# Kernel optimization log

Hardware: AMD Instinct MI355X
Metric: run time of the kernel (lower is better)

## Reference

```python
import jax, jax.numpy as jnp
import numpy as np

N, E, P = 50000, 800000, 500000
NODE_IN, HIDDEN, EDGE_IN = 128, 256, 16


def setup_inputs() -> dict:
    key = jax.random.key(0)
    ks = jax.random.split(key, 16)
    s = lambda k, shape, fan_in: jax.random.normal(k, shape, jnp.float32) * (1.0 / np.sqrt(fan_in))
    return {
        "x": jax.random.normal(ks[0], (N, NODE_IN), jnp.float32),
        "edge_index": jax.random.randint(ks[1], (2, E), 0, N),
        "edge_u": jax.random.randint(ks[2], (P,), 0, N),
        "edge_v": jax.random.randint(ks[3], (P,), 0, N),
        "edge_attr": jax.random.normal(ks[4], (P, EDGE_IN), jnp.float32),
        "log_exposure": jax.random.normal(ks[5], (P,), jnp.float32),
        # conv1: lin_l (on mean-aggregated neighbors, with bias), lin_r (on root, no bias)
        "Wl1": s(ks[6], (HIDDEN, NODE_IN), NODE_IN),
        "bl1": jnp.zeros((HIDDEN,), jnp.float32),
        "Wr1": s(ks[7], (HIDDEN, NODE_IN), NODE_IN),
        # conv2
        "Wl2": s(ks[8], (HIDDEN, HIDDEN), HIDDEN),
        "bl2": jnp.zeros((HIDDEN,), jnp.float32),
        "Wr2": s(ks[9], (HIDDEN, HIDDEN), HIDDEN),
        # edge MLP: Linear(2*hidden+edge_in, hidden) -> ReLU -> Linear(hidden, 1)
        "W1": s(ks[10], (HIDDEN, 2 * HIDDEN + EDGE_IN), 2 * HIDDEN + EDGE_IN),
        "b1": jnp.zeros((HIDDEN,), jnp.float32),
        "W2": s(ks[11], (1, HIDDEN), HIDDEN),
        "b2": jnp.zeros((1,), jnp.float32),
    }


def sage_conv(x, src, dst, Wl, bl, Wr):
    # PyG SAGEConv, mean aggregation: out = lin_l(mean_{j in N(i)} x_j) + lin_r(x_i)
    n = x.shape[0]
    agg = jax.ops.segment_sum(x[src], dst, num_segments=n)          # [N, F]
    cnt = jax.ops.segment_sum(jnp.ones((src.shape[0],), x.dtype), dst, num_segments=n)
    agg = agg / jnp.maximum(cnt, 1.0)[:, None]
    return agg @ Wl.T + bl + x @ Wr.T


def reference(x, edge_index, edge_u, edge_v, edge_attr, log_exposure,
              Wl1, bl1, Wr1, Wl2, bl2, Wr2, W1, b1, W2, b2):
    src, dst = edge_index[0], edge_index[1]
    # eval mode: dropout is identity
    h = jax.nn.relu(sage_conv(x, src, dst, Wl1, bl1, Wr1))
    h = jax.nn.relu(sage_conv(h, src, dst, Wl2, bl2, Wr2))
    z = jnp.concatenate([h[edge_u], h[edge_v], edge_attr], axis=1)  # [P, 2H+Ein]
    s = (jax.nn.relu(z @ W1.T + b1) @ W2.T + b2)[:, 0]              # [P]
    return log_exposure + s
```

## Files before the change

kernel.cpp:

```cpp
#include <hip/hip_runtime.h>


typedef float f32x4 __attribute__((ext_vector_type(4)));
typedef float f32x2 __attribute__((ext_vector_type(2)));
typedef __bf16 bf16x8 __attribute__((ext_vector_type(8)));

__device__ __forceinline__ unsigned short f2b(float f) {
    unsigned u = __float_as_uint(f);
    u = u + 0x7fffu + ((u >> 16) & 1u);
    return (unsigned short)(u >> 16);
}
__device__ __forceinline__ float b2f(unsigned short s) {
    return __uint_as_float(((unsigned)s) << 16);
}
__device__ __forceinline__ float blo(unsigned x) { return b2f((unsigned short)(x & 0xffffu)); }
__device__ __forceinline__ float bhi(unsigned x) { return b2f((unsigned short)(x >> 16)); }
__device__ __forceinline__ unsigned padd(unsigned a, unsigned b) {
    float lo = __uint_as_float(a << 16) + __uint_as_float(b << 16);
    float hi = __uint_as_float(a & 0xffff0000u) + __uint_as_float(b & 0xffff0000u);
    return (__float_as_uint(hi) & 0xffff0000u) | (__float_as_uint(lo) >> 16);
}
__device__ __forceinline__ int swz(int r, int g) { return (g + (r >> 1)) & 3; }
__device__ __forceinline__ unsigned char f2f8(float v) {
    return (unsigned char)(__builtin_amdgcn_cvt_pk_fp8_f32(v, v, 0, false) & 0xff);
}


__global__ void k_count(const int* __restrict__ dst, int* __restrict__ cnt, int E) {
    int e = blockIdx.x * 256 + threadIdx.x;
    if (e < E) atomicAdd(&cnt[dst[e]], 1);
}

__global__ __launch_bounds__(1024) void k_scan(int* __restrict__ cnt_cursor,
                                               int* __restrict__ row_ptr, int n) {
    __shared__ int wsum[16];
    __shared__ int carry;
    int t = threadIdx.x, lane = t & 63, w = t >> 6;
    if (t == 0) carry = 0;
    __syncthreads();
    int nch = (n + 1023) >> 10;
    for (int ch = 0; ch < nch; ++ch) {
        int i = (ch << 10) + t;
        int v = (i < n) ? cnt_cursor[i] : 0;
        int s = v;
        #pragma unroll
        for (int off = 1; off < 64; off <<= 1) {
            int u = __shfl_up(s, off);
            if (lane >= off) s += u;
        }
        if (lane == 63) wsum[w] = s;
        __syncthreads();
        int wpre = 0;
        for (int j = 0; j < w; ++j) wpre += wsum[j];
        int incl = s + wpre;
        int base = carry;
        if (i < n) { int ex = base + incl - v; row_ptr[i] = ex; cnt_cursor[i] = ex; }
        __syncthreads();
        if (t == 1023) carry = base + incl;
    }
    __syncthreads();
    if (t == 0) row_ptr[n] = carry;
}

__global__ void k_scatter(const int* __restrict__ src, const int* __restrict__ dst,
                          int* __restrict__ cursor, int* __restrict__ bucket, int E) {
    int e = blockIdx.x * 256 + threadIdx.x;
    if (e < E) {
        int p = atomicAdd(&cursor[dst[e]], 1);
        bucket[p] = src[e];
    }
}


__global__ void k_convert_weights(const float* __restrict__ Wl1, const float* __restrict__ Wr1,
                                  const float* __restrict__ Wl2, const float* __restrict__ Wr2,
                                  const float* __restrict__ W1, const float* __restrict__ b1,
                                  unsigned short* __restrict__ Wc1,
                                  unsigned short* __restrict__ Wc2,
                                  unsigned short* __restrict__ W1g,
                                  unsigned short* __restrict__ WaF) {
    int idx = blockIdx.x * 256 + threadIdx.x;
    if (idx < 65536) {
        int c = idx >> 13, j = (idx >> 5) & 255, kk = idx & 31;
        float v = (c < 4) ? Wl1[j * 128 + c * 32 + kk] : Wr1[j * 128 + (c - 4) * 32 + kk];
        Wc1[idx] = f2b(v);
    } else if (idx < 65536 + 131072) {
        int i2 = idx - 65536;
        int c = i2 >> 13, j = (i2 >> 5) & 255, kk = i2 & 31;
        float v = (c < 8) ? Wl2[j * 256 + c * 32 + kk] : Wr2[j * 256 + (c - 8) * 32 + kk];
        Wc2[i2] = f2b(v);
    } else if (idx < 65536 + 131072 + 131072) {
        int i3 = idx - 65536 - 131072;
        int c = i3 >> 14, j = (i3 >> 5) & 511, kk = i3 & 31;
        float v = (j < 256) ? W1[(size_t)j * 528 + c * 32 + kk]
                            : W1[(size_t)(j - 256) * 528 + 256 + c * 32 + kk];
        W1g[i3] = f2b(v);
    } else if (idx < 65536 + 131072 + 131072 + 8192) {
        int i4 = idx - 65536 - 131072 - 131072;
        int mi = i4 >> 9, l = (i4 >> 3) & 63, j = i4 & 7;
        int m = mi * 16 + (l & 15);
        int k = (l >> 4) * 8 + j;
        float v = (k < 16) ? W1[(size_t)m * 528 + 512 + k] : (k == 16 ? b1[m] : 0.f);
        WaF[i4] = f2b(v);
    }
}

__global__ void k_xconvert(const float* __restrict__ in, unsigned short* __restrict__ xb,
                           unsigned char* __restrict__ xf8, int n) {
    int j = (blockIdx.x * 256 + threadIdx.x) * 2;
    if (j < n) {
        float a = in[j], b = in[j + 1];
        xb[j] = f2b(a); xb[j + 1] = f2b(b);
        unsigned p = __builtin_amdgcn_cvt_pk_fp8_f32(a, b, 0, false);
        *reinterpret_cast<unsigned short*>(xf8 + j) = (unsigned short)(p & 0xffffu);
    }
}


__device__ __forceinline__ void accf8(uint2 v, float* s) {
    f32x2 p0 = __builtin_amdgcn_cvt_pk_f32_fp8(v.x, false);
    f32x2 p1 = __builtin_amdgcn_cvt_pk_f32_fp8(v.x, true);
    f32x2 p2 = __builtin_amdgcn_cvt_pk_f32_fp8(v.y, false);
    f32x2 p3 = __builtin_amdgcn_cvt_pk_f32_fp8(v.y, true);
    s[0] += p0.x; s[1] += p0.y; s[2] += p1.x; s[3] += p1.y;
    s[4] += p2.x; s[5] += p2.y; s[6] += p3.x; s[7] += p3.y;
}

__global__ __launch_bounds__(256) void k_agg_x(const unsigned char* __restrict__ xf8,
                                               const int* __restrict__ row_ptr,
                                               const int* __restrict__ bucket,
                                               unsigned short* __restrict__ agg, int Nn) {
    int node = blockIdx.x * 4 + (threadIdx.x >> 6);
    if (node >= Nn) return;
    int lane = threadIdx.x & 63;
    int q = lane >> 4, c = lane & 15;
    int beg = row_ptr[node], end = row_ptr[node + 1];
    int len = end - beg;
    int lo = beg + ((len * q) >> 2);
    int hi = beg + ((len * (q + 1)) >> 2);
    float s[8] = {0.f,0.f,0.f,0.f,0.f,0.f,0.f,0.f};
    const unsigned char* xp = xf8 + c * 8;
    int e = lo;
    for (; e + 4 <= hi; e += 4) {
        int b0 = bucket[e], b1 = bucket[e + 1], b2 = bucket[e + 2], b3 = bucket[e + 3];
        uint2 v0 = *reinterpret_cast<const uint2*>(xp + (size_t)b0 * 128);
        uint2 v1 = *reinterpret_cast<const uint2*>(xp + (size_t)b1 * 128);
        uint2 v2 = *reinterpret_cast<const uint2*>(xp + (size_t)b2 * 128);
        uint2 v3 = *reinterpret_cast<const uint2*>(xp + (size_t)b3 * 128);
        accf8(v0, s); accf8(v1, s); accf8(v2, s); accf8(v3, s);
    }
    for (; e < hi; ++e)
        accf8(*reinterpret_cast<const uint2*>(xp + (size_t)bucket[e] * 128), s);
    #pragma unroll
    for (int j = 0; j < 8; ++j) {
        s[j] += __shfl_xor(s[j], 16);
        s[j] += __shfl_xor(s[j], 32);
    }
    if (q == 0) {
        float sc = 1.0f / (float)(len > 1 ? len : 1);
        uint4 o;
        o.x = (unsigned)f2b(s[0]*sc) | ((unsigned)f2b(s[1]*sc) << 16);
        o.y = (unsigned)f2b(s[2]*sc) | ((unsigned)f2b(s[3]*sc) << 16);
        o.z = (unsigned)f2b(s[4]*sc) | ((unsigned)f2b(s[5]*sc) << 16);
        o.w = (unsigned)f2b(s[6]*sc) | ((unsigned)f2b(s[7]*sc) << 16);
        *reinterpret_cast<uint4*>(agg + (size_t)node * 128 + c * 8) = o;
    }
}

__global__ __launch_bounds__(256) void k_agg_h(const unsigned char* __restrict__ hf8,
                                               const int* __restrict__ row_ptr,
                                               const int* __restrict__ bucket,
                                               unsigned short* __restrict__ agg, int Nn) {
    int node = blockIdx.x * 4 + (threadIdx.x >> 6);
    if (node >= Nn) return;
    int lane = threadIdx.x & 63;
    int g = lane >> 5, c = lane & 31;
    int beg = row_ptr[node], end = row_ptr[node + 1];
    int len = end - beg;
    int lo = beg + ((len * g) >> 1);
    int hi = beg + ((len * (g + 1)) >> 1);
    float s[8] = {0.f,0.f,0.f,0.f,0.f,0.f,0.f,0.f};
    const unsigned char* hp = hf8 + c * 8;
    int e = lo;
    for (; e + 4 <= hi; e += 4) {
        int b0 = bucket[e], b1 = bucket[e + 1], b2 = bucket[e + 2], b3 = bucket[e + 3];
        uint2 v0 = *reinterpret_cast<const uint2*>(hp + (size_t)b0 * 256);
        uint2 v1 = *reinterpret_cast<const uint2*>(hp + (size_t)b1 * 256);
        uint2 v2 = *reinterpret_cast<const uint2*>(hp + (size_t)b2 * 256);
        uint2 v3 = *reinterpret_cast<const uint2*>(hp + (size_t)b3 * 256);
        accf8(v0, s); accf8(v1, s); accf8(v2, s); accf8(v3, s);
    }
    for (; e < hi; ++e)
        accf8(*reinterpret_cast<const uint2*>(hp + (size_t)bucket[e] * 256), s);
    #pragma unroll
    for (int j = 0; j < 8; ++j) s[j] += __shfl_xor(s[j], 32);
    if (g == 0) {
        float sc = 1.0f / (float)(len > 1 ? len : 1);
        uint4 o;
        o.x = (unsigned)f2b(s[0]*sc) | ((unsigned)f2b(s[1]*sc) << 16);
        o.y = (unsigned)f2b(s[2]*sc) | ((unsigned)f2b(s[3]*sc) << 16);
        o.z = (unsigned)f2b(s[4]*sc) | ((unsigned)f2b(s[5]*sc) << 16);
        o.w = (unsigned)f2b(s[6]*sc) | ((unsigned)f2b(s[7]*sc) << 16);
        *reinterpret_cast<uint4*>(agg + (size_t)node * 256 + c * 8) = o;
    }
}


__global__ __launch_bounds__(256) void k_conv_gemm(const unsigned short* __restrict__ Aagg,
                                                   const unsigned short* __restrict__ Aself,
                                                   const unsigned short* __restrict__ Wck,
                                                   const float* __restrict__ bias,
                                                   unsigned short* __restrict__ Hout,
                                                   unsigned char* __restrict__ Hf8,
                                                   int Nn, int F) {
    __shared__ __align__(16) unsigned short zt[128 * 32];
    __shared__ __align__(16) unsigned short wt[128 * 32];
    const int t = threadIdx.x;
    const int lane = t & 63, w = t >> 6;
    const int wm = w >> 1, wn = w & 1;
    const int node0 = blockIdx.x * 128;
    const int colh = blockIdx.y;
    const int half = F >> 5, nchunks = F >> 4;

    f32x4 acc[4][4];
    #pragma unroll
    for (int i = 0; i < 4; ++i)
        #pragma unroll
        for (int j = 0; j < 4; ++j) acc[i][j] = (f32x4){0.f, 0.f, 0.f, 0.f};

    for (int c = 0; c < nchunks; ++c) {
        __syncthreads();
        const unsigned short* Asrc = (c < half) ? Aagg : Aself;
        const int ccol = ((c < half) ? c : c - half) * 32;
        #pragma unroll
        for (int p = 0; p < 2; ++p) {
            int fc = t + p * 256;
            int row = fc >> 2, seg = fc & 3;
            int node = node0 + row; if (node >= Nn) node = Nn - 1;
            uint4 v = *reinterpret_cast<const uint4*>(Asrc + (size_t)node * F + ccol + seg * 8);
            *reinterpret_cast<uint4*>(&zt[row * 32 + swz(row, seg) * 8]) = v;
        }
        const unsigned short* Wsrc = Wck + ((size_t)c * 256 + colh * 128) * 32;
        #pragma unroll
        for (int p = 0; p < 2; ++p) {
            int fc = t + p * 256;
            int row = fc >> 2, seg = fc & 3;
            *reinterpret_cast<uint4*>(&wt[row * 32 + swz(row, seg) * 8]) =
                *reinterpret_cast<const uint4*>(Wsrc + fc * 8);
        }
        __syncthreads();
        bf16x8 a[4], b[4];
        const int q = lane >> 4;
        #pragma unroll
        for (int mi = 0; mi < 4; ++mi) {
            int R = wm * 64 + mi * 16 + (lane & 15);
            a[mi] = *reinterpret_cast<const bf16x8*>(&zt[R * 32 + swz(R, q) * 8]);
        }
        #pragma unroll
        for (int ni = 0; ni < 4; ++ni) {
            int R = wn * 64 + ni * 16 + (lane & 15);
            b[ni] = *reinterpret_cast<const bf16x8*>(&wt[R * 32 + swz(R, q) * 8]);
        }
        #pragma unroll
        for (int mi = 0; mi < 4; ++mi)
            #pragma unroll
            for (int ni = 0; ni < 4; ++ni)
                acc[mi][ni] = __builtin_amdgcn_mfma_f32_16x16x32_bf16(a[mi], b[ni], acc[mi][ni], 0, 0, 0);
    }

    #pragma unroll
    for (int mi = 0; mi < 4; ++mi)
        #pragma unroll
        for (int ni = 0; ni < 4; ++ni) {
            int col = colh * 128 + wn * 64 + ni * 16 + (lane & 15);
            float bia = bias[col];
            #pragma unroll
            for (int r = 0; r < 4; ++r) {
                int row = node0 + wm * 64 + mi * 16 + ((lane >> 4) << 2) + r;
                if (row < Nn) {
                    float v = acc[mi][ni][r] + bia;
                    v = v > 0.f ? v : 0.f;
                    Hout[(size_t)row * 256 + col] = f2b(v);
                    if (Hf8) Hf8[(size_t)row * 256 + col] = f2f8(v);
                }
            }
        }
}


__global__ __launch_bounds__(256) void k_gemm_g(const unsigned short* __restrict__ A,
                                                const unsigned short* __restrict__ Wck,
                                                unsigned short* __restrict__ Gout,
                                                int Nn) {
    __shared__ __align__(16) unsigned short zt[128 * 32];
    __shared__ __align__(16) unsigned short wt[128 * 32];
    const int t = threadIdx.x;
    const int lane = t & 63, w = t >> 6;
    const int wm = w >> 1, wn = w & 1;
    const int node0 = blockIdx.x * 128;
    const int colg = blockIdx.y;

    f32x4 acc[4][4];
    #pragma unroll
    for (int i = 0; i < 4; ++i)
        #pragma unroll
        for (int j = 0; j < 4; ++j) acc[i][j] = (f32x4){0.f, 0.f, 0.f, 0.f};

    for (int c = 0; c < 8; ++c) {
        __syncthreads();
        #pragma unroll
        for (int p = 0; p < 2; ++p) {
            int fc = t + p * 256;
            int row = fc >> 2, seg = fc & 3;
            int node = node0 + row; if (node >= Nn) node = Nn - 1;
            uint4 v = *reinterpret_cast<const uint4*>(A + (size_t)node * 256 + c * 32 + seg * 8);
            *reinterpret_cast<uint4*>(&zt[row * 32 + swz(row, seg) * 8]) = v;
        }
        const unsigned short* Wsrc = Wck + ((size_t)c * 512 + colg * 128) * 32;
        #pragma unroll
        for (int p = 0; p < 2; ++p) {
            int fc = t + p * 256;
            int row = fc >> 2, seg = fc & 3;
            *reinterpret_cast<uint4*>(&wt[row * 32 + swz(row, seg) * 8]) =
                *reinterpret_cast<const uint4*>(Wsrc + fc * 8);
        }
        __syncthreads();
        bf16x8 a[4], b[4];
        const int q = lane >> 4;
        #pragma unroll
        for (int mi = 0; mi < 4; ++mi) {
            int R = wm * 64 + mi * 16 + (lane & 15);
            a[mi] = *reinterpret_cast<const bf16x8*>(&zt[R * 32 + swz(R, q) * 8]);
        }
        #pragma unroll
        for (int ni = 0; ni < 4; ++ni) {
            int R = wn * 64 + ni * 16 + (lane & 15);
            b[ni] = *reinterpret_cast<const bf16x8*>(&wt[R * 32 + swz(R, q) * 8]);
        }
        #pragma unroll
        for (int mi = 0; mi < 4; ++mi)
            #pragma unroll
            for (int ni = 0; ni < 4; ++ni)
                acc[mi][ni] = __builtin_amdgcn_mfma_f32_16x16x32_bf16(a[mi], b[ni], acc[mi][ni], 0, 0, 0);
    }

    #pragma unroll
    for (int mi = 0; mi < 4; ++mi)
        #pragma unroll
        for (int ni = 0; ni < 4; ++ni) {
            int col = colg * 128 + wn * 64 + ni * 16 + (lane & 15);
            #pragma unroll
            for (int r = 0; r < 4; ++r) {
                int row = node0 + wm * 64 + mi * 16 + ((lane >> 4) << 2) + r;
                if (row < Nn)
                    Gout[(size_t)row * 512 + col] = f2b(acc[mi][ni][r]);
            }
        }
}


__global__ __launch_bounds__(256, 6) void k_edge(const unsigned short* __restrict__ G2,
                                                 const float* __restrict__ attr,
                                                 const int* __restrict__ eu,
                                                 const int* __restrict__ ev,
                                                 const uint4* __restrict__ WaF,
                                                 const float* __restrict__ W2,
                                                 const float* __restrict__ b2,
                                                 const float* __restrict__ logexp,
                                                 float* __restrict__ out, int P) {
    __shared__ __align__(16) unsigned short attrT[64 * 40];
    __shared__ __align__(16) unsigned short gt[64 * 132];
    __shared__ float w2s[256];
    __shared__ int euv[128];
    const int t = threadIdx.x;
    const int lane = t & 63, w = t >> 6;
    const int base = blockIdx.x * 64;

    {
        int e = t >> 2, seg = t & 3;
        int eg = base + e; if (eg >= P) eg = P - 1;
        const float4 f = *reinterpret_cast<const float4*>(attr + (size_t)eg * 16 + seg * 4);
        uint2 o;
        o.x = (unsigned)f2b(f.x) | ((unsigned)f2b(f.y) << 16);
        o.y = (unsigned)f2b(f.z) | ((unsigned)f2b(f.w) << 16);
        *reinterpret_cast<uint2*>(&attrT[e * 40 + seg * 4]) = o;
    }
    if (t < 64) {
        uint2 z0; z0.x = 0x3f80u; z0.y = 0u;
        *reinterpret_cast<uint2*>(&attrT[t * 40 + 16]) = z0;
        uint2 z1; z1.x = 0u; z1.y = 0u;
        *reinterpret_cast<uint2*>(&attrT[t * 40 + 20]) = z1;
        uint4 z2; z2.x = z2.y = z2.z = z2.w = 0u;
        *reinterpret_cast<uint4*>(&attrT[t * 40 + 24]) = z2;
    }
    if (t < 128) {
        int e = t >> 1;
        int eg = base + e; if (eg >= P) eg = P - 1;
        euv[t] = (t & 1) ? ev[eg] : eu[eg];
    }
    w2s[t] = W2[t];
    __syncthreads();

    const int el = lane & 15, q = lane >> 4;
    const int grow = w * 16 + el;
    const bf16x8 bfrag = *reinterpret_cast<const bf16x8*>(&attrT[grow * 40 + q * 8]);

    float s = 0.f;
    #pragma unroll
    for (int p = 0; p < 2; ++p) {
        {
            const int sub = lane >> 4, c = lane & 15;
            #pragma unroll
            for (int i = 0; i < 4; ++i) {
                int le = w * 16 + i * 4 + sub;
                int u = euv[2 * le], v = euv[2 * le + 1];
                uint4 a = *reinterpret_cast<const uint4*>(G2 + (size_t)u * 512 + p * 128 + c * 8);
                uint4 b = *reinterpret_cast<const uint4*>(G2 + (size_t)v * 512 + 256 + p * 128 + c * 8);
                uint4 o;
                o.x = padd(a.x, b.x);
                o.y = padd(a.y, b.y);
                o.z = padd(a.z, b.z);
                o.w = padd(a.w, b.w);
                *reinterpret_cast<uint4*>(&gt[le * 132 + c * 8]) = o;
            }
        }
        #pragma unroll
        for (int m = 0; m < 8; ++m) {
            const int mi = p * 8 + m;
            const bf16x8 af = *reinterpret_cast<const bf16x8*>(&WaF[mi * 64 + lane]);
            f32x4 acc = __builtin_amdgcn_mfma_f32_16x16x32_bf16(af, bfrag, (f32x4){0.f,0.f,0.f,0.f}, 0, 0, 0);
            const uint2 g2v = *reinterpret_cast<const uint2*>(&gt[grow * 132 + m * 16 + q * 4]);
            const float4 w2v = *reinterpret_cast<const float4*>(&w2s[mi * 16 + q * 4]);
            float y0 = acc[0] + blo(g2v.x);
            float y1 = acc[1] + bhi(g2v.x);
            float y2 = acc[2] + blo(g2v.y);
            float y3 = acc[3] + bhi(g2v.y);
            s += (y0 > 0.f ? y0 : 0.f) * w2v.x;
            s += (y1 > 0.f ? y1 : 0.f) * w2v.y;
            s += (y2 > 0.f ? y2 : 0.f) * w2v.z;
            s += (y3 > 0.f ? y3 : 0.f) * w2v.w;
        }
        if (p == 0) __syncthreads();
    }
    s += __shfl_xor(s, 16);
    s += __shfl_xor(s, 32);
    int eg = base + grow;
    if (q == 0 && eg < P)
        out[eg] = logexp[eg] + b2[0] + s;
}


extern "C" void kernel_launch(void* const* d_in, const int* in_sizes, int n_in,
                              void* d_out, int out_size, void* d_ws, size_t ws_size,
                              hipStream_t stream) {
    const float* x      = (const float*)d_in[0];
    const int*   eidx   = (const int*)d_in[1];
    const int*   eu     = (const int*)d_in[2];
    const int*   ev     = (const int*)d_in[3];
    const float* attr   = (const float*)d_in[4];
    const float* logexp = (const float*)d_in[5];
    const float* Wl1    = (const float*)d_in[6];
    const float* bl1    = (const float*)d_in[7];
    const float* Wr1    = (const float*)d_in[8];
    const float* Wl2    = (const float*)d_in[9];
    const float* bl2    = (const float*)d_in[10];
    const float* Wr2    = (const float*)d_in[11];
    const float* W1     = (const float*)d_in[12];
    const float* b1     = (const float*)d_in[13];
    const float* W2     = (const float*)d_in[14];
    const float* b2     = (const float*)d_in[15];
    float* out = (float*)d_out;

    const int N = in_sizes[0] / 128;
    const int E = in_sizes[1] / 2;
    const int P = in_sizes[2];
    const int* src = eidx;
    const int* dst = eidx + E;

    char* ws = (char*)d_ws;
    size_t off = 0;
    auto alloc = [&](size_t bytes) -> void* {
        off = (off + 255) & ~(size_t)255;
        void* p = ws + off;
        off += bytes;
        return p;
    };
    int* row_ptr = (int*)alloc((size_t)(N + 1) * 4);
    int* cursor  = (int*)alloc((size_t)N * 4);
    int* bucket  = (int*)alloc((size_t)E * 4);
    unsigned short* h1 = (unsigned short*)alloc((size_t)N * 256 * 2);
    unsigned short* h2 = (unsigned short*)alloc((size_t)N * 256 * 2);
    char* shared_base = (char*)alloc((size_t)N * 512 * 2);
    unsigned short* xb   = (unsigned short*)shared_base;
    unsigned short* agg1 = (unsigned short*)(shared_base + (size_t)N * 128 * 2);
    unsigned short* agg2 = (unsigned short*)(shared_base + (size_t)N * 256 * 2);
    unsigned short* G2   = (unsigned short*)shared_base;
    unsigned char* xf8  = (unsigned char*)alloc((size_t)N * 128);
    unsigned char* h1f8 = (unsigned char*)alloc((size_t)N * 256);
    unsigned short* Wc1  = (unsigned short*)alloc((size_t)65536 * 2);
    unsigned short* Wc2  = (unsigned short*)alloc((size_t)131072 * 2);
    unsigned short* W1g  = (unsigned short*)alloc((size_t)131072 * 2);
    unsigned short* WaF  = (unsigned short*)alloc((size_t)8192 * 2);

    hipMemsetAsync(cursor, 0, (size_t)N * 4, stream);
    k_count<<<(E + 255) / 256, 256, 0, stream>>>(dst, cursor, E);
    k_scan<<<1, 1024, 0, stream>>>(cursor, row_ptr, N);
    k_scatter<<<(E + 255) / 256, 256, 0, stream>>>(src, dst, cursor, bucket, E);
    k_convert_weights<<<(65536 + 131072 + 131072 + 8192 + 255) / 256, 256, 0, stream>>>(
        Wl1, Wr1, Wl2, Wr2, W1, b1, Wc1, Wc2, W1g, WaF);
    k_xconvert<<<(N * 64 + 255) / 256, 256, 0, stream>>>(x, xb, xf8, N * 128);

    k_agg_x<<<(N + 3) / 4, 256, 0, stream>>>(xf8, row_ptr, bucket, agg1, N);
    dim3 gconv((N + 127) / 128, 2);
    k_conv_gemm<<<gconv, 256, 0, stream>>>(agg1, xb, Wc1, bl1, h1, h1f8, N, 128);
    k_agg_h<<<(N + 3) / 4, 256, 0, stream>>>(h1f8, row_ptr, bucket, agg2, N);
    k_conv_gemm<<<gconv, 256, 0, stream>>>(agg2, h1, Wc2, bl2, h2, (unsigned char*)nullptr, N, 256);

    dim3 gg((N + 127) / 128, 4);
    k_gemm_g<<<gg, 256, 0, stream>>>(h2, W1g, G2, N);
    k_edge<<<(P + 63) / 64, 256, 0, stream>>>(G2, attr, eu, ev, (const uint4*)WaF,
                                              W2, b2, logexp, out, P);
}
```

Baseline: 503.4 us.

## Store per-node edge-MLP projections as fp8 and parallelize scan block prefix

The per-node projection table G2 used by the edge MLP is now written as fp8 instead of bf16. This halves the bytes gathered per edge endpoint in the edge kernel, which is dominated by random gathers over 500k edges. The u and v halves are kept separately in shared memory and unpacked with hardware fp8-to-f32 conversion, replacing the bf16 packed add. It also replaces the serial per-wave prefix loop in the scan kernel with a shuffle-based scan over the wave sums. The cost is lower precision in the pre-activation sum, which risks larger numerical error.

```diff
diff --git a/kernel.cpp b/kernel.cpp
--- a/kernel.cpp
+++ b/kernel.cpp
@@ -13,13 +13,6 @@
 __device__ __forceinline__ float b2f(unsigned short s) {
     return __uint_as_float(((unsigned)s) << 16);
 }
-__device__ __forceinline__ float blo(unsigned x) { return b2f((unsigned short)(x & 0xffffu)); }
-__device__ __forceinline__ float bhi(unsigned x) { return b2f((unsigned short)(x >> 16)); }
-__device__ __forceinline__ unsigned padd(unsigned a, unsigned b) {
-    float lo = __uint_as_float(a << 16) + __uint_as_float(b << 16);
-    float hi = __uint_as_float(a & 0xffff0000u) + __uint_as_float(b & 0xffff0000u);
-    return (__float_as_uint(hi) & 0xffff0000u) | (__float_as_uint(lo) >> 16);
-}
 __device__ __forceinline__ int swz(int r, int g) { return (g + (r >> 1)) & 3; }
 __device__ __forceinline__ unsigned char f2f8(float v) {
     return (unsigned char)(__builtin_amdgcn_cvt_pk_fp8_f32(v, v, 0, false) & 0xff);
@@ -34,7 +27,7 @@
 __global__ __launch_bounds__(1024) void k_scan(int* __restrict__ cnt_cursor,
                                                int* __restrict__ row_ptr, int n) {
     __shared__ int wsum[16];
-    __shared__ int carry;
+    __shared__ int carry, wtot;
     int t = threadIdx.x, lane = t & 63, w = t >> 6;
     if (t == 0) carry = 0;
     __syncthreads();
@@ -50,13 +43,23 @@
         }
         if (lane == 63) wsum[w] = s;
         __syncthreads();
-        int wpre = 0;
-        for (int j = 0; j < w; ++j) wpre += wsum[j];
-        int incl = s + wpre;
+        if (t < 16) {
+            int vv = wsum[t];
+            int s2 = vv;
+            #pragma unroll
+            for (int off = 1; off < 16; off <<= 1) {
+                int u = __shfl_up(s2, off);
+                if (t >= off) s2 += u;
+            }
+            wsum[t] = s2 - vv;
+            if (t == 15) wtot = s2;
+        }
+        __syncthreads();
         int base = carry;
+        int incl = s + wsum[w];
         if (i < n) { int ex = base + incl - v; row_ptr[i] = ex; cnt_cursor[i] = ex; }
         __syncthreads();
-        if (t == 1023) carry = base + incl;
+        if (t == 0) carry = base + wtot;
     }
     __syncthreads();
     if (t == 0) row_ptr[n] = carry;
@@ -290,7 +293,7 @@
 
 __global__ __launch_bounds__(256) void k_gemm_g(const unsigned short* __restrict__ A,
                                                 const unsigned short* __restrict__ Wck,
-                                                unsigned short* __restrict__ Gout,
+                                                unsigned char* __restrict__ Gout,
                                                 int Nn) {
     __shared__ __align__(16) unsigned short zt[128 * 32];
     __shared__ __align__(16) unsigned short wt[128 * 32];
@@ -353,13 +356,13 @@
             for (int r = 0; r < 4; ++r) {
                 int row = node0 + wm * 64 + mi * 16 + ((lane >> 4) << 2) + r;
                 if (row < Nn)
-                    Gout[(size_t)row * 512 + col] = f2b(acc[mi][ni][r]);
+                    Gout[(size_t)row * 512 + col] = f2f8(acc[mi][ni][r]);
             }
         }
 }
 
 
-__global__ __launch_bounds__(256, 6) void k_edge(const unsigned short* __restrict__ G2,
+__global__ __launch_bounds__(256, 6) void k_edge(const unsigned char* __restrict__ G2,
                                                  const float* __restrict__ attr,
                                                  const int* __restrict__ eu,
                                                  const int* __restrict__ ev,
@@ -369,7 +372,7 @@
                                                  const float* __restrict__ logexp,
                                                  float* __restrict__ out, int P) {
     __shared__ __align__(16) unsigned short attrT[64 * 40];
-    __shared__ __align__(16) unsigned short gt[64 * 132];
+    __shared__ __align__(16) unsigned char gt[64 * 264];
     __shared__ float w2s[256];
     __shared__ int euv[128];
     const int t = threadIdx.x;
@@ -414,14 +417,10 @@
             for (int i = 0; i < 4; ++i) {
                 int le = w * 16 + i * 4 + sub;
                 int u = euv[2 * le], v = euv[2 * le + 1];
-                uint4 a = *reinterpret_cast<const uint4*>(G2 + (size_t)u * 512 + p * 128 + c * 8);
-                uint4 b = *reinterpret_cast<const uint4*>(G2 + (size_t)v * 512 + 256 + p * 128 + c * 8);
-                uint4 o;
-                o.x = padd(a.x, b.x);
-                o.y = padd(a.y, b.y);
-                o.z = padd(a.z, b.z);
-                o.w = padd(a.w, b.w);
-                *reinterpret_cast<uint4*>(&gt[le * 132 + c * 8]) = o;
+                uint2 a = *reinterpret_cast<const uint2*>(G2 + (size_t)u * 512 + p * 128 + c * 8);
+                uint2 b = *reinterpret_cast<const uint2*>(G2 + (size_t)v * 512 + 256 + p * 128 + c * 8);
+                *reinterpret_cast<uint2*>(&gt[le * 264 + c * 8]) = a;
+                *reinterpret_cast<uint2*>(&gt[le * 264 + 128 + c * 8]) = b;
             }
         }
         #pragma unroll
@@ -429,12 +428,17 @@
             const int mi = p * 8 + m;
             const bf16x8 af = *reinterpret_cast<const bf16x8*>(&WaF[mi * 64 + lane]);
             f32x4 acc = __builtin_amdgcn_mfma_f32_16x16x32_bf16(af, bfrag, (f32x4){0.f,0.f,0.f,0.f}, 0, 0, 0);
-            const uint2 g2v = *reinterpret_cast<const uint2*>(&gt[grow * 132 + m * 16 + q * 4]);
+            const unsigned gu4 = *reinterpret_cast<const unsigned*>(&gt[grow * 264 + m * 16 + q * 4]);
+            const unsigned gv4 = *reinterpret_cast<const unsigned*>(&gt[grow * 264 + 128 + m * 16 + q * 4]);
             const float4 w2v = *reinterpret_cast<const float4*>(&w2s[mi * 16 + q * 4]);
-            float y0 = acc[0] + blo(g2v.x);
-            float y1 = acc[1] + bhi(g2v.x);
-            float y2 = acc[2] + blo(g2v.y);
-            float y3 = acc[3] + bhi(g2v.y);
+            f32x2 ulo = __builtin_amdgcn_cvt_pk_f32_fp8(gu4, false);
+            f32x2 uhi = __builtin_amdgcn_cvt_pk_f32_fp8(gu4, true);
+            f32x2 vlo = __builtin_amdgcn_cvt_pk_f32_fp8(gv4, false);
+            f32x2 vhi = __builtin_amdgcn_cvt_pk_f32_fp8(gv4, true);
+            float y0 = acc[0] + ulo.x + vlo.x;
+            float y1 = acc[1] + ulo.y + vlo.y;
+            float y2 = acc[2] + uhi.x + vhi.x;
+            float y3 = acc[3] + uhi.y + vhi.y;
             s += (y0 > 0.f ? y0 : 0.f) * w2v.x;
             s += (y1 > 0.f ? y1 : 0.f) * w2v.y;
             s += (y2 > 0.f ? y2 : 0.f) * w2v.z;
@@ -494,7 +498,7 @@
     unsigned short* xb   = (unsigned short*)shared_base;
     unsigned short* agg1 = (unsigned short*)(shared_base + (size_t)N * 128 * 2);
     unsigned short* agg2 = (unsigned short*)(shared_base + (size_t)N * 256 * 2);
-    unsigned short* G2   = (unsigned short*)shared_base;
+    unsigned char*  G2f8 = (unsigned char*)shared_base;
     unsigned char* xf8  = (unsigned char*)alloc((size_t)N * 128);
     unsigned char* h1f8 = (unsigned char*)alloc((size_t)N * 256);
     unsigned short* Wc1  = (unsigned short*)alloc((size_t)65536 * 2);
@@ -517,7 +521,7 @@
     k_conv_gemm<<<gconv, 256, 0, stream>>>(agg2, h1, Wc2, bl2, h2, (unsigned char*)nullptr, N, 256);
 
     dim3 gg((N + 127) / 128, 4);
-    k_gemm_g<<<gg, 256, 0, stream>>>(h2, W1g, G2, N);
-    k_edge<<<(P + 63) / 64, 256, 0, stream>>>(G2, attr, eu, ev, (const uint4*)WaF,
+    k_gemm_g<<<gg, 256, 0, stream>>>(h2, W1g, G2f8, N);
+    k_edge<<<(P + 63) / 64, 256, 0, stream>>>(G2f8, attr, eu, ev, (const uint4*)WaF,
                                               W2, b2, logexp, out, P);
 }
```

Result: faster. 479.6 us (-4.7%).
